# Kernel tuning notes

Measured on AMD Instinct MI355X. Metric: run time of the kernel, lower is better.

## Reference

```python
import jax, jax.numpy as jnp
import numpy as np

B, L, N, D = 128, 256, 64, 1024  # batch, text_len, img_num, feat size (text=obj=place=D)


def masked_softmax(logits, mask=None):
    # matches MaskedSoftmax(dim=1): softmax over last axis, then renormalize by mask
    dist = jax.nn.softmax(logits, axis=-1)
    if mask is None:
        return dist
    dist = dist * mask
    return dist / jnp.sum(dist, axis=-1, keepdims=True)


def setup_inputs() -> dict:
    key = jax.random.key(0)
    ks = jax.random.split(key, 32)
    s = lambda d: 1.0 / np.sqrt(d)
    inp = {
        'text_feat': jax.random.normal(ks[0], (B, D), jnp.float32),
        'text_feats': jax.random.normal(ks[1], (B, L, D), jnp.float32),
        'img_object_feat': jax.random.normal(ks[2], (B, D), jnp.float32),
        'img_object_feats': jax.random.normal(ks[3], (B, N, D), jnp.float32),
        'img_place_feat': jax.random.normal(ks[4], (B, D), jnp.float32),
        'img_place_feats': jax.random.normal(ks[5], (B, N, D), jnp.float32),
        'src_mask': (jax.random.uniform(ks[6], (B, L)) < 0.9).astype(jnp.float32).at[:, 0].set(1.0),
        # score vectors (nn.Linear(D,1,bias=False))
        'v_to': jax.random.uniform(ks[7], (D,), jnp.float32, -s(D), s(D)),
        'v_tp': jax.random.uniform(ks[8], (D,), jnp.float32, -s(D), s(D)),
        'v_io': jax.random.uniform(ks[9], (D,), jnp.float32, -s(D), s(D)),
        'v_ip': jax.random.uniform(ks[10], (D,), jnp.float32, -s(D), s(D)),
        # cross-modal projections (bias=False), torch layout [out,in]
        'W_t2o': jax.random.uniform(ks[11], (D, D), jnp.float32, -s(D), s(D)),
        'W_t2p': jax.random.uniform(ks[12], (D, D), jnp.float32, -s(D), s(D)),
        'W_o2t': jax.random.uniform(ks[13], (D, D), jnp.float32, -s(D), s(D)),
        'W_p2t': jax.random.uniform(ks[14], (D, D), jnp.float32, -s(D), s(D)),
        # self projections with bias
        'W_oo': jax.random.uniform(ks[15], (D, D), jnp.float32, -s(D), s(D)),
        'b_oo': jax.random.uniform(ks[16], (D,), jnp.float32, -s(D), s(D)),
        'W_pp': jax.random.uniform(ks[17], (D, D), jnp.float32, -s(D), s(D)),
        'b_pp': jax.random.uniform(ks[18], (D,), jnp.float32, -s(D), s(D)),
        'W_tot': jax.random.uniform(ks[19], (D, D), jnp.float32, -s(D), s(D)),
        'b_tot': jax.random.uniform(ks[20], (D,), jnp.float32, -s(D), s(D)),
        'W_tpt': jax.random.uniform(ks[21], (D, D), jnp.float32, -s(D), s(D)),
        'b_tpt': jax.random.uniform(ks[22], (D,), jnp.float32, -s(D), s(D)),
        # output linear: in = 2*D + D + D = 4D
        'W_out': jax.random.uniform(ks[23], (D, 4 * D), jnp.float32, -s(4 * D), s(4 * D)),
        'b_out': jax.random.uniform(ks[24], (D,), jnp.float32, -s(4 * D), s(4 * D)),
    }
    return inp


def _text_att_ctx(text_feat, img_feats, W_img2text, W_text, b_text, v):
    # additive attention of text over image regions
    e = jnp.tanh(jnp.einsum('bnd,td->bnt', img_feats, W_img2text)
                 + (text_feat @ W_text.T + b_text)[:, None, :])
    scores = jnp.einsum('bnt,t->bn', e, v)
    dist = masked_softmax(scores)
    return jnp.einsum('bn,bnd->bd', dist, img_feats)


def _img_att_ctx(img_feat, text_feats, W_text2img, W_img, b_img, v, mask):
    e = jnp.tanh(jnp.einsum('bld,id->bli', text_feats, W_text2img)
                 + (img_feat @ W_img.T + b_img)[:, None, :])
    scores = jnp.einsum('bli,i->bl', e, v)
    dist = masked_softmax(scores, mask)
    return jnp.einsum('bl,bld->bd', dist, text_feats)


def reference(text_feat, text_feats, img_object_feat, img_object_feats, img_place_feat,
              img_place_feats, src_mask, v_to, v_tp, v_io, v_ip, W_t2o, W_t2p, W_o2t,
              W_p2t, W_oo, b_oo, W_pp, b_pp, W_tot, b_tot, W_tpt, b_tpt, W_out, b_out):
    img_object_context = _text_att_ctx(text_feat, img_object_feats, W_o2t, W_tot, b_tot, v_to)
    img_place_context = _text_att_ctx(text_feat, img_place_feats, W_p2t, W_tpt, b_tpt, v_tp)
    text_object_context = _img_att_ctx(img_object_feat, text_feats, W_t2o, W_oo, b_oo, v_io, src_mask)
    text_place_context = _img_att_ctx(img_place_feat, text_feats, W_t2p, W_pp, b_pp, v_ip, src_mask)
    combined = jnp.concatenate([img_object_context, img_place_context,
                                text_object_context, text_place_context], axis=1)
    # dropout is identity at inference
    return combined @ W_out.T + b_out
```

## Files before the change

### kernel.cpp

```cpp
#include <hip/hip_runtime.h>
#include <hip/hip_bf16.h>

typedef __attribute__((ext_vector_type(8))) short bf16x8;
typedef __attribute__((ext_vector_type(4))) float f32x4;
typedef __attribute__((ext_vector_type(2))) long lx2;

__device__ __forceinline__ uint pack_bf16x2(float a, float b) {
    __hip_bfloat162 p = __float22bfloat162_rn(make_float2(a, b));
    union { __hip_bfloat162 h; uint u; } c; c.h = p; return c.u;
}

__device__ __forceinline__ float fast_tanh(float x) {
    float e = __expf(2.f * x);
    return 1.f - 2.f * __builtin_amdgcn_rcpf(e + 1.f);
}

__device__ __forceinline__ float wredmax(float v) {
    #pragma unroll
    for (int o = 32; o; o >>= 1) v = fmaxf(v, __shfl_xor(v, o, 64));
    return v;
}
__device__ __forceinline__ float wredsum(float v) {
    #pragma unroll
    for (int o = 32; o; o >>= 1) v += __shfl_xor(v, o, 64);
    return v;
}

__device__ __forceinline__ void gload16(const void* g, void* l) {
    __builtin_amdgcn_global_load_lds(
        (const __attribute__((address_space(1))) void*)g,
        (__attribute__((address_space(3))) void*)l, 16, 0, 0);
}

struct Cvt8Tab {
    const float* src[8];
    uchar* dst[8];
    unsigned cum[9];
};
struct CvtTab {
    const float* src[8];
    ushort* dst[8];
    unsigned cum[9];
};

__device__ __forceinline__ uint pk8(float4 v) {
    int r = __builtin_amdgcn_cvt_pk_fp8_f32(v.x, v.y, 0, false);
    r = __builtin_amdgcn_cvt_pk_fp8_f32(v.z, v.w, r, true);
    return (uint)r;
}

__global__ void cvt_all(Cvt8Tab t8, unsigned total8, CvtTab tb, unsigned totalb) {
    unsigned stride = gridDim.x * blockDim.x;
    unsigned total = total8 + totalb;
    for (unsigned i = blockIdx.x * blockDim.x + threadIdx.x; i < total; i += stride) {
        if (i < total8) {
            int j = 0;
            while (i >= t8.cum[j + 1]) ++j;
            unsigned o = i - t8.cum[j];
            unsigned row = o >> 6, c = o & 63, tt = c >> 2, pp = c & 3;
            const float* s0 = t8.src[j] + (size_t)row * 1024 + tt * 64 + pp * 8;
            float4 a0 = *(const float4*)(s0);
            float4 a1 = *(const float4*)(s0 + 4);
            float4 b0 = *(const float4*)(s0 + 32);
            float4 b1 = *(const float4*)(s0 + 36);
            uint4 ov;
            ov.x = pk8(a0); ov.y = pk8(a1); ov.z = pk8(b0); ov.w = pk8(b1);
            *reinterpret_cast<uint4*>(t8.dst[j] + (size_t)o * 16) = ov;
        } else {
            unsigned ii = i - total8;
            int j = 0;
            while (ii >= tb.cum[j + 1]) ++j;
            unsigned off = ii - tb.cum[j];
            float4 v = reinterpret_cast<const float4*>(tb.src[j])[off];
            uint2 o;
            o.x = pack_bf16x2(v.x, v.y);
            o.y = pack_bf16x2(v.z, v.w);
            reinterpret_cast<uint2*>(tb.dst[j])[off] = o;
        }
    }
}

struct PArgs {
    const uchar* A[2];
    const uchar* Wa[2];
    const uchar* Wb[2];
    const float* qa[2];
    const float* qb[2];
    const float* va[2];
    const float* vb[2];
    float* oa[2];
    float* ob[2];
};

__global__ __launch_bounds__(512, 1) void gemm_pipe8(PArgs Pi, PArgs Pt)
{
    extern __shared__ char smem[];

    const int tid = threadIdx.x;
    const int lane = tid & 63, wv = tid >> 6;
    const int wr = wv >> 2, wc = wv & 3;
    const int lrow = lane & 15, lk = lane >> 4;

    int id = blockIdx.x;
    const PArgs* P;
    int x, y, nmul, nbadd, bshift, brshift;
    if (id < 256) {
        P = &Pi; x = id & 63; y = id >> 6;
        nmul = 256; nbadd = 128; bshift = 6; brshift = 5;
    } else {
        P = &Pt; id -= 256; x = id & 127; y = id >> 7;
        nmul = 128; nbadd = 0; bshift = 8; brshift = 7;
    }
    const int br = x >> brshift;
    const int m0 = (x & ((1 << brshift) - 1)) << 8;
    const int na = y * nmul;
    const int nb = na + nbadd;

    const uchar* A  = P->A[br];
    const uchar* Wa = P->Wa[br];
    const uchar* Wb = P->Wb[br];

    const int rr = tid >> 2;
    const int c  = (tid & 3) ^ ((tid >> 3) & 3);
    const uchar* sA0 = A  + (size_t)(m0 + rr) * 1024 + c * 16;
    const uchar* sA1 = A  + (size_t)(m0 + 128 + rr) * 1024 + c * 16;
    const uchar* sW0 = Wa + (size_t)(na + rr) * 1024 + c * 16;
    const uchar* sW1 = Wb + (size_t)(nb + rr) * 1024 + c * 16;

    auto stage = [&](int t, int d) {
        char* b = smem + d * 32768 + tid * 16;
        size_t k = (size_t)t * 64;
        gload16(sA0 + k, b);
        gload16(sA1 + k, b + 8192);
        gload16(sW0 + k, b + 16384);
        gload16(sW1 + k, b + 24576);
    };

    auto rdA = [&](int d, int mi) -> lx2 {
        int row = wr * 128 + mi * 16 + lrow;
        return *(const lx2*)(smem + d * 32768 + row * 64 +
                             ((lk ^ ((row >> 1) & 3)) << 4));
    };
    auto rdB = [&](int d, int ni) -> lx2 {
        int row = wc * 64 + ni * 16 + lrow;
        return *(const lx2*)(smem + d * 32768 + 16384 + row * 64 +
                             ((lk ^ ((row >> 1) & 3)) << 4));
    };

    f32x4 acc[8][4];
    #pragma unroll
    for (int i = 0; i < 8; ++i)
        #pragma unroll
        for (int j = 0; j < 4; ++j) { f32x4 z = {0.f,0.f,0.f,0.f}; acc[i][j] = z; }

    stage(0, 0);
    asm volatile("s_waitcnt vmcnt(0)" ::: "memory");
    __syncthreads();

    auto body = [&](int t, int cur, int nxt, bool pf) {
        lx2 af[4], bfr[4];
        if (pf) stage(t + 1, nxt);
        #pragma unroll
        for (int ni = 0; ni < 4; ++ni) bfr[ni] = rdB(cur, ni);
        #pragma unroll
        for (int mi = 0; mi < 4; ++mi) af[mi] = rdA(cur, mi);
        __builtin_amdgcn_s_setprio(1);
        #pragma unroll
        for (int mi = 0; mi < 4; ++mi)
            #pragma unroll
            for (int ni = 0; ni < 4; ++ni) {
                acc[mi][ni] = __builtin_amdgcn_mfma_f32_16x16x32_fp8_fp8(af[mi][0], bfr[ni][0], acc[mi][ni], 0, 0, 0);
                acc[mi][ni] = __builtin_amdgcn_mfma_f32_16x16x32_fp8_fp8(af[mi][1], bfr[ni][1], acc[mi][ni], 0, 0, 0);
            }
        __builtin_amdgcn_s_setprio(0);
        #pragma unroll
        for (int mi = 0; mi < 4; ++mi) af[mi] = rdA(cur, mi + 4);
        __builtin_amdgcn_s_setprio(1);
        #pragma unroll
        for (int mi = 0; mi < 4; ++mi)
            #pragma unroll
            for (int ni = 0; ni < 4; ++ni) {
                acc[mi + 4][ni] = __builtin_amdgcn_mfma_f32_16x16x32_fp8_fp8(af[mi][0], bfr[ni][0], acc[mi + 4][ni], 0, 0, 0);
                acc[mi + 4][ni] = __builtin_amdgcn_mfma_f32_16x16x32_fp8_fp8(af[mi][1], bfr[ni][1], acc[mi + 4][ni], 0, 0, 0);
            }
        __builtin_amdgcn_s_setprio(0);
        asm volatile("s_waitcnt vmcnt(0)" ::: "memory");
        __syncthreads();
    };

    #pragma unroll 1
    for (int tt = 0; tt < 8; ++tt) {
        body(2 * tt,     0, 1, true);
        body(2 * tt + 1, 1, 0, tt < 7);
    }

    const float* qsrc = (wc < 2) ? P->qa[br] : P->qb[br];
    const float* vsrc = (wc < 2) ? P->va[br] : P->vb[br];
    float* osrc       = (wc < 2) ? P->oa[br] : P->ob[br];
    const int nbase0 = ((wc < 2) ? na : nb) + (wc & 1) * 64;
    #pragma unroll
    for (int mi = 0; mi < 8; ++mi) {
        int mbase = m0 + wr * 128 + mi * 16;
        int bb = mbase >> bshift;
        const float* qrow = qsrc + (size_t)bb * 1024;
        float part[4] = {0.f, 0.f, 0.f, 0.f};
        #pragma unroll
        for (int ni = 0; ni < 4; ++ni) {
            int nn = nbase0 + ni * 16 + lrow;
            float qn = qrow[nn], vn = vsrc[nn];
            #pragma unroll
            for (int r2 = 0; r2 < 4; ++r2)
                part[r2] += fast_tanh(acc[mi][ni][r2] + qn) * vn;
        }
        #pragma unroll
        for (int off = 1; off < 16; off <<= 1)
            #pragma unroll
            for (int r2 = 0; r2 < 4; ++r2)
                part[r2] += __shfl_xor(part[r2], off, 64);
        if (lrow == 0) {
            #pragma unroll
            for (int r2 = 0; r2 < 4; ++r2)
                atomicAdd(&osrc[mbase + lk * 4 + r2], part[r2]);
        }
    }
}

struct QArgs {
    const ushort* A[4];
    const ushort* W[4];
    const float* bias[4];
    float* out[4];
};

__global__ __launch_bounds__(256, 2) void gemm_q(QArgs Q, int kchunk)
{
    __shared__ char smemq[32768];
    char* As = smemq;
    char* Ws = smemq + 16384;

    const int tid = threadIdx.x;
    const int lane = tid & 63, wv = tid >> 6, wr = wv >> 1, wc = wv & 1;
    const int lrow = lane & 15, lk = lane >> 4;
    const int n0 = blockIdx.y << 7;
    const int nkt = kchunk >> 6;
    const int ktbase = blockIdx.z * nkt;

    const ushort* A = Q.A[blockIdx.x];
    const ushort* W = Q.W[blockIdx.x];

    f32x4 acc[4][4];
    #pragma unroll
    for (int i = 0; i < 4; ++i)
        #pragma unroll
        for (int j = 0; j < 4; ++j) { f32x4 z = {0.f,0.f,0.f,0.f}; acc[i][j] = z; }

    const int srow = tid >> 3;
    const int g = (tid & 7) ^ (srow & 7);
    const ushort* pA = A + (size_t)srow * 1024 + (size_t)ktbase * 64 + g * 8;
    const ushort* pW = W + (size_t)(n0 + srow) * 1024 + (size_t)ktbase * 64 + g * 8;

    for (int t = 0; t < nkt; ++t) {
        #pragma unroll
        for (int j = 0; j < 4; ++j)
            gload16(pA + (size_t)j * 32768 + (size_t)t * 64, As + j * 4096 + tid * 16);
        #pragma unroll
        for (int j = 0; j < 4; ++j)
            gload16(pW + (size_t)j * 32768 + (size_t)t * 64, Ws + j * 4096 + tid * 16);
        __syncthreads();
        #pragma unroll
        for (int ks = 0; ks < 2; ++ks) {
            bf16x8 af[4], bfr[4];
            const int q = ks * 4 + lk;
            #pragma unroll
            for (int mi = 0; mi < 4; ++mi) {
                int row = wr * 64 + mi * 16 + lrow;
                af[mi] = *(const bf16x8*)(As + row * 128 + ((q ^ (row & 7)) << 4));
            }
            #pragma unroll
            for (int ni = 0; ni < 4; ++ni) {
                int row = wc * 64 + ni * 16 + lrow;
                bfr[ni] = *(const bf16x8*)(Ws + row * 128 + ((q ^ (row & 7)) << 4));
            }
            #pragma unroll
            for (int mi = 0; mi < 4; ++mi)
                #pragma unroll
                for (int ni = 0; ni < 4; ++ni)
                    acc[mi][ni] = __builtin_amdgcn_mfma_f32_16x16x32_bf16(af[mi], bfr[ni], acc[mi][ni], 0, 0, 0);
        }
        __syncthreads();
    }

    float* out = Q.out[blockIdx.x];
    const float* bias = Q.bias[blockIdx.x];
    #pragma unroll
    for (int mi = 0; mi < 4; ++mi) {
        int mrow0 = wr * 64 + mi * 16 + lk * 4;
        #pragma unroll
        for (int ni = 0; ni < 4; ++ni) {
            int n = n0 + wc * 64 + ni * 16 + lrow;
            float bv = (blockIdx.z == 0) ? bias[n] : 0.f;
            #pragma unroll
            for (int r = 0; r < 4; ++r)
                atomicAdd(&out[(size_t)(mrow0 + r) * 1024 + n], acc[mi][ni][r] + bv);
        }
    }
}

__global__ __launch_bounds__(256, 2) void gemm_fin(
    const ushort* A, const ushort* W, const float* bias, float* out, int K, int kchunk)
{
    __shared__ char smemf[32768];
    char* As = smemf;
    char* Ws = smemf + 16384;

    const int tid = threadIdx.x;
    const int lane = tid & 63, wv = tid >> 6, wr = wv >> 1, wc = wv & 1;
    const int lrow = lane & 15, lk = lane >> 4;
    const int n0 = blockIdx.y << 7;
    const int nkt = kchunk >> 6;
    const int ktbase = blockIdx.z * nkt;

    f32x4 acc[4][4];
    #pragma unroll
    for (int i = 0; i < 4; ++i)
        #pragma unroll
        for (int j = 0; j < 4; ++j) { f32x4 z = {0.f,0.f,0.f,0.f}; acc[i][j] = z; }

    const int srow = tid >> 3;
    const int g = (tid & 7) ^ (srow & 7);
    const ushort* pA = A + (size_t)srow * K + ktbase * 64 + g * 8;
    const ushort* pW = W + (size_t)(n0 + srow) * K + ktbase * 64 + g * 8;

    for (int t = 0; t < nkt; ++t) {
        #pragma unroll
        for (int j = 0; j < 4; ++j)
            gload16(pA + (size_t)j * 32 * K + (size_t)t * 64, As + j * 4096 + tid * 16);
        #pragma unroll
        for (int j = 0; j < 4; ++j)
            gload16(pW + (size_t)j * 32 * K + (size_t)t * 64, Ws + j * 4096 + tid * 16);
        __syncthreads();
        #pragma unroll
        for (int ks = 0; ks < 2; ++ks) {
            bf16x8 af[4], bfr[4];
            const int q = ks * 4 + lk;
            #pragma unroll
            for (int mi = 0; mi < 4; ++mi) {
                int row = wr * 64 + mi * 16 + lrow;
                af[mi] = *(const bf16x8*)(As + row * 128 + ((q ^ (row & 7)) << 4));
            }
            #pragma unroll
            for (int ni = 0; ni < 4; ++ni) {
                int row = wc * 64 + ni * 16 + lrow;
                bfr[ni] = *(const bf16x8*)(Ws + row * 128 + ((q ^ (row & 7)) << 4));
            }
            #pragma unroll
            for (int mi = 0; mi < 4; ++mi)
                #pragma unroll
                for (int ni = 0; ni < 4; ++ni)
                    acc[mi][ni] = __builtin_amdgcn_mfma_f32_16x16x32_bf16(af[mi], bfr[ni], acc[mi][ni], 0, 0, 0);
        }
        __syncthreads();
    }

    #pragma unroll
    for (int mi = 0; mi < 4; ++mi) {
        int mrow0 = wr * 64 + mi * 16 + lk * 4;
        #pragma unroll
        for (int ni = 0; ni < 4; ++ni) {
            int n = n0 + wc * 64 + ni * 16 + lrow;
            float bv = (blockIdx.z == 0) ? bias[n] : 0.f;
            #pragma unroll
            for (int r = 0; r < 4; ++r)
                atomicAdd(&out[(size_t)(mrow0 + r) * 1024 + n], acc[mi][ni][r] + bv);
        }
    }
}

__global__ void softmax_ctx(const float* __restrict__ tf,
                            const float* __restrict__ iof, const float* __restrict__ ipf,
                            const float* __restrict__ sc_to, const float* __restrict__ sc_tp,
                            const float* __restrict__ sc_io, const float* __restrict__ sc_ip,
                            const float* __restrict__ mask, ushort* __restrict__ combined)
{
    int b = blockIdx.x, y = blockIdx.y;
    int tid = threadIdx.x, lane = tid & 63, wv = tid >> 6;
    if (y >= 2) {
        int brn = y - 2;
        const float* A  = brn ? ipf : iof;
        const float* sc = brn ? sc_ip : sc_io;
        __shared__ float dist[64];
        if (tid < 64) {
            float s  = sc[b * 64 + tid];
            float mx = wredmax(s);
            float e  = __expf(s - mx);
            float sm = wredsum(e);
            dist[tid] = e / sm;
        }
        __syncthreads();
        int d0 = tid * 4;
        float a0 = 0, a1 = 0, a2 = 0, a3 = 0;
        const float* base = A + (size_t)b * 64 * 1024 + d0;
        #pragma unroll 4
        for (int n = 0; n < 64; ++n) {
            float w = dist[n];
            float4 t = *(const float4*)(base + (size_t)n * 1024);
            a0 += w * t.x; a1 += w * t.y; a2 += w * t.z; a3 += w * t.w;
        }
        uint2 o;
        o.x = pack_bf16x2(a0, a1);
        o.y = pack_bf16x2(a2, a3);
        *(uint2*)(combined + (size_t)b * 4096 + brn * 1024 + d0) = o;
    } else {
        __shared__ float d3[256], d4[256], red[8];
        float s3 = sc_to[b * 256 + tid], s4 = sc_tp[b * 256 + tid], m = mask[b * 256 + tid];
        float m3 = wredmax(s3), m4 = wredmax(s4);
        if (lane == 0) { red[wv] = m3; red[4 + wv] = m4; }
        __syncthreads();
        m3 = fmaxf(fmaxf(red[0], red[1]), fmaxf(red[2], red[3]));
        m4 = fmaxf(fmaxf(red[4], red[5]), fmaxf(red[6], red[7]));
        float e3 = __expf(s3 - m3) * m, e4 = __expf(s4 - m4) * m;
        float t3 = wredsum(e3), t4 = wredsum(e4);
        __syncthreads();
        if (lane == 0) { red[wv] = t3; red[4 + wv] = t4; }
        __syncthreads();
        t3 = red[0] + red[1] + red[2] + red[3];
        t4 = red[4] + red[5] + red[6] + red[7];
        d3[tid] = e3 / t3; d4[tid] = e4 / t4;
        __syncthreads();
        int d0 = y * 512 + tid * 2;
        float a0 = 0, a1 = 0, c0 = 0, c1 = 0;
        const float* base = tf + (size_t)b * 256 * 1024 + d0;
        #pragma unroll 4
        for (int l = 0; l < 256; ++l) {
            float w3 = d3[l], w4 = d4[l];
            float2 t = *(const float2*)(base + (size_t)l * 1024);
            a0 += w3 * t.x; a1 += w3 * t.y;
            c0 += w4 * t.x; c1 += w4 * t.y;
        }
        *(uint*)(combined + (size_t)b * 4096 + 2048 + d0) = pack_bf16x2(a0, a1);
        *(uint*)(combined + (size_t)b * 4096 + 3072 + d0) = pack_bf16x2(c0, c1);
    }
}

extern "C" void kernel_launch(void* const* d_in, const int* in_sizes, int n_in,
                              void* d_out, int out_size, void* d_ws, size_t ws_size,
                              hipStream_t stream) {
    const float* text_feat        = (const float*)d_in[0];
    const float* text_feats       = (const float*)d_in[1];
    const float* img_object_feat  = (const float*)d_in[2];
    const float* img_object_feats = (const float*)d_in[3];
    const float* img_place_feat   = (const float*)d_in[4];
    const float* img_place_feats  = (const float*)d_in[5];
    const float* src_mask         = (const float*)d_in[6];
    const float* v_to  = (const float*)d_in[7];
    const float* v_tp  = (const float*)d_in[8];
    const float* v_io  = (const float*)d_in[9];
    const float* v_ip  = (const float*)d_in[10];
    const float* W_t2o = (const float*)d_in[11];
    const float* W_t2p = (const float*)d_in[12];
    const float* W_o2t = (const float*)d_in[13];
    const float* W_p2t = (const float*)d_in[14];
    const float* W_oo  = (const float*)d_in[15];
    const float* b_oo  = (const float*)d_in[16];
    const float* W_pp  = (const float*)d_in[17];
    const float* b_pp  = (const float*)d_in[18];
    const float* W_tot = (const float*)d_in[19];
    const float* b_tot = (const float*)d_in[20];
    const float* W_tpt = (const float*)d_in[21];
    const float* b_tpt = (const float*)d_in[22];
    const float* W_out = (const float*)d_in[23];
    const float* b_out = (const float*)d_in[24];

    char* p = (char*)d_ws;
    auto alloc = [&](size_t bytes) { char* r = p; p += (bytes + 255) & ~(size_t)255; return r; };
    ushort* wq_oo  = (ushort*)alloc((size_t)1024 * 1024 * 2);
    ushort* wq_pp  = (ushort*)alloc((size_t)1024 * 1024 * 2);
    ushort* wq_tot = (ushort*)alloc((size_t)1024 * 1024 * 2);
    ushort* wq_tpt = (ushort*)alloc((size_t)1024 * 1024 * 2);
    ushort* wb_out = (ushort*)alloc((size_t)1024 * 4096 * 2);
    ushort* tfq_bf  = (ushort*)alloc((size_t)128 * 1024 * 2);
    ushort* iofq_bf = (ushort*)alloc((size_t)128 * 1024 * 2);
    ushort* ipfq_bf = (ushort*)alloc((size_t)128 * 1024 * 2);
    uchar* w8_t2o = (uchar*)alloc((size_t)1024 * 1024);
    uchar* w8_t2p = (uchar*)alloc((size_t)1024 * 1024);
    uchar* w8_o2t = (uchar*)alloc((size_t)1024 * 1024);
    uchar* w8_p2t = (uchar*)alloc((size_t)1024 * 1024);
    uchar* tf8  = (uchar*)alloc((size_t)32768 * 1024);
    uchar* iof8 = (uchar*)alloc((size_t)8192 * 1024);
    uchar* ipf8 = (uchar*)alloc((size_t)8192 * 1024);
    float* q_tot = (float*)alloc((size_t)128 * 1024 * 4);
    float* q_tpt = (float*)alloc((size_t)128 * 1024 * 4);
    float* q_oo  = (float*)alloc((size_t)128 * 1024 * 4);
    float* q_pp  = (float*)alloc((size_t)128 * 1024 * 4);
    float* scores = (float*)alloc((size_t)(8192 * 2 + 32768 * 2) * 4);
    float* sc_io = scores, *sc_ip = scores + 8192, *sc_to = scores + 16384, *sc_tp = scores + 49152;
    ushort* comb_bf = (ushort*)alloc((size_t)128 * 4096 * 2);

    Cvt8Tab t8;
    const float* s8[7] = { W_t2o, W_t2p, W_o2t, W_p2t, text_feats, img_object_feats, img_place_feats };
    uchar* d8[7] = { w8_t2o, w8_t2p, w8_o2t, w8_p2t, tf8, iof8, ipf8 };
    unsigned n16[7] = { 65536, 65536, 65536, 65536, 2097152, 524288, 524288 };
    unsigned cum8 = 0;
    for (int i = 0; i < 7; ++i) { t8.src[i] = s8[i]; t8.dst[i] = d8[i]; t8.cum[i] = cum8; cum8 += n16[i]; }
    t8.src[7] = nullptr; t8.dst[7] = nullptr; t8.cum[7] = cum8; t8.cum[8] = cum8;

    CvtTab tb;
    const float* sb[8] = { W_oo, W_pp, W_tot, W_tpt, W_out, text_feat, img_object_feat, img_place_feat };
    ushort* db[8] = { wq_oo, wq_pp, wq_tot, wq_tpt, wb_out, tfq_bf, iofq_bf, ipfq_bf };
    unsigned nb4[8] = { 262144, 262144, 262144, 262144, 1048576, 32768, 32768, 32768 };
    unsigned cumb = 0;
    for (int i = 0; i < 8; ++i) { tb.src[i] = sb[i]; tb.dst[i] = db[i]; tb.cum[i] = cumb; cumb += nb4[i]; }
    tb.cum[8] = cumb;
    cvt_all<<<4096, 256, 0, stream>>>(t8, cum8, tb, cumb);

    hipMemsetAsync(q_tot, 0, (size_t)4 * 524288 + 327680, stream);
    hipMemsetAsync(d_out, 0, (size_t)128 * 1024 * 4, stream);

    QArgs qa;
    qa.A[0] = tfq_bf;  qa.W[0] = wq_tot; qa.bias[0] = b_tot; qa.out[0] = q_tot;
    qa.A[1] = tfq_bf;  qa.W[1] = wq_tpt; qa.bias[1] = b_tpt; qa.out[1] = q_tpt;
    qa.A[2] = iofq_bf; qa.W[2] = wq_oo;  qa.bias[2] = b_oo;  qa.out[2] = q_oo;
    qa.A[3] = ipfq_bf; qa.W[3] = wq_pp;  qa.bias[3] = b_pp;  qa.out[3] = q_pp;
    gemm_q<<<dim3(4, 8, 4), 256, 0, stream>>>(qa, 256);

    PArgs pi;
    pi.A[0] = iof8;   pi.Wa[0] = w8_o2t; pi.Wb[0] = w8_o2t;
    pi.qa[0] = q_tot; pi.qb[0] = q_tot;  pi.va[0] = v_to; pi.vb[0] = v_to;
    pi.oa[0] = sc_io; pi.ob[0] = sc_io;
    pi.A[1] = ipf8;   pi.Wa[1] = w8_p2t; pi.Wb[1] = w8_p2t;
    pi.qa[1] = q_tpt; pi.qb[1] = q_tpt;  pi.va[1] = v_tp; pi.vb[1] = v_tp;
    pi.oa[1] = sc_ip; pi.ob[1] = sc_ip;

    PArgs pt;
    pt.A[0] = tf8;    pt.Wa[0] = w8_t2o; pt.Wb[0] = w8_t2p;
    pt.qa[0] = q_oo;  pt.qb[0] = q_pp;   pt.va[0] = v_io; pt.vb[0] = v_ip;
    pt.oa[0] = sc_to; pt.ob[0] = sc_tp;
    pt.A[1] = pt.A[0]; pt.Wa[1] = pt.Wa[0]; pt.Wb[1] = pt.Wb[0];
    pt.qa[1] = pt.qa[0]; pt.qb[1] = pt.qb[0]; pt.va[1] = pt.va[0]; pt.vb[1] = pt.vb[0];
    pt.oa[1] = pt.oa[0]; pt.ob[1] = pt.ob[0];

    gemm_pipe8<<<dim3(1280), 512, 65536, stream>>>(pi, pt);

    softmax_ctx<<<dim3(128, 4), 256, 0, stream>>>(
        text_feats, img_object_feats, img_place_feats,
        sc_to, sc_tp, sc_io, sc_ip, src_mask, comb_bf);

    gemm_fin<<<dim3(1, 8, 16), 256, 0, stream>>>(comb_bf, wb_out, b_out, (float*)d_out, 4096, 256);
}
```

Before: 270.1 us.

## Halve FP8 GEMM M-tile to 128 rows and fold memsets into convert kernel

The fused FP8 score GEMM now uses 256-thread blocks with a 128x256 tile (4 waves in a 2x2 arrangement, each computing 64x128) instead of 512-thread blocks with a 256x256 tile. This doubles the grid and allows two blocks per CU through launch bounds and a smaller LDS footprint, aiming at better occupancy and latency hiding at the cost of lower operand reuse per block. Separately, the two hipMemsetAsync calls are removed and their zeroing is folded into the cvt_all kernel's grid-stride loop, which saves launch overhead.

Result: faster. 246.7 us (median of 2 runs) (-8.6%).

```diff
diff --git a/kernel.cpp b/kernel.cpp
--- a/kernel.cpp
+++ b/kernel.cpp
@@ -49,9 +49,10 @@
     return (uint)r;
 }
 
-__global__ void cvt_all(Cvt8Tab t8, unsigned total8, CvtTab tb, unsigned totalb) {
+__global__ void cvt_all(Cvt8Tab t8, unsigned total8, CvtTab tb, unsigned totalb,
+                        uint4* z1, unsigned n1, uint4* z2, unsigned n2) {
     unsigned stride = gridDim.x * blockDim.x;
-    unsigned total = total8 + totalb;
+    unsigned total = total8 + totalb + n1 + n2;
     for (unsigned i = blockIdx.x * blockDim.x + threadIdx.x; i < total; i += stride) {
         if (i < total8) {
             int j = 0;
@@ -66,7 +67,7 @@
             uint4 ov;
             ov.x = pk8(a0); ov.y = pk8(a1); ov.z = pk8(b0); ov.w = pk8(b1);
             *reinterpret_cast<uint4*>(t8.dst[j] + (size_t)o * 16) = ov;
-        } else {
+        } else if (i < total8 + totalb) {
             unsigned ii = i - total8;
             int j = 0;
             while (ii >= tb.cum[j + 1]) ++j;
@@ -76,6 +77,11 @@
             o.x = pack_bf16x2(v.x, v.y);
             o.y = pack_bf16x2(v.z, v.w);
             reinterpret_cast<uint2*>(tb.dst[j])[off] = o;
+        } else {
+            unsigned ii = i - total8 - totalb;
+            uint4 zz = {0u, 0u, 0u, 0u};
+            if (ii < n1) z1[ii] = zz;
+            else z2[ii - n1] = zz;
         }
     }
 }
@@ -92,27 +98,27 @@
     float* ob[2];
 };
 
-__global__ __launch_bounds__(512, 1) void gemm_pipe8(PArgs Pi, PArgs Pt)
+__global__ __launch_bounds__(256, 2) void gemm_pipe8(PArgs Pi, PArgs Pt)
 {
     extern __shared__ char smem[];
 
     const int tid = threadIdx.x;
     const int lane = tid & 63, wv = tid >> 6;
-    const int wr = wv >> 2, wc = wv & 3;
+    const int wr = wv >> 1, wc = wv & 1;
     const int lrow = lane & 15, lk = lane >> 4;
 
     int id = blockIdx.x;
     const PArgs* P;
     int x, y, nmul, nbadd, bshift, brshift;
-    if (id < 256) {
-        P = &Pi; x = id & 63; y = id >> 6;
-        nmul = 256; nbadd = 128; bshift = 6; brshift = 5;
+    if (id < 512) {
+        P = &Pi; x = id & 127; y = id >> 7;
+        nmul = 256; nbadd = 128; bshift = 6; brshift = 6;
     } else {
-        P = &Pt; id -= 256; x = id & 127; y = id >> 7;
-        nmul = 128; nbadd = 0; bshift = 8; brshift = 7;
+        P = &Pt; id -= 512; x = id & 255; y = id >> 8;
+        nmul = 128; nbadd = 0; bshift = 8; brshift = 8;
     }
     const int br = x >> brshift;
-    const int m0 = (x & ((1 << brshift) - 1)) << 8;
+    const int m0 = (x & ((1 << brshift) - 1)) << 7;
     const int na = y * nmul;
     const int nb = na + nbadd;
 
@@ -123,35 +129,39 @@
     const int rr = tid >> 2;
     const int c  = (tid & 3) ^ ((tid >> 3) & 3);
     const uchar* sA0 = A  + (size_t)(m0 + rr) * 1024 + c * 16;
-    const uchar* sA1 = A  + (size_t)(m0 + 128 + rr) * 1024 + c * 16;
+    const uchar* sA1 = A  + (size_t)(m0 + 64 + rr) * 1024 + c * 16;
     const uchar* sW0 = Wa + (size_t)(na + rr) * 1024 + c * 16;
-    const uchar* sW1 = Wb + (size_t)(nb + rr) * 1024 + c * 16;
+    const uchar* sW1 = Wa + (size_t)(na + 64 + rr) * 1024 + c * 16;
+    const uchar* sW2 = Wb + (size_t)(nb + rr) * 1024 + c * 16;
+    const uchar* sW3 = Wb + (size_t)(nb + 64 + rr) * 1024 + c * 16;
 
     auto stage = [&](int t, int d) {
-        char* b = smem + d * 32768 + tid * 16;
+        char* b = smem + d * 24576 + tid * 16;
         size_t k = (size_t)t * 64;
         gload16(sA0 + k, b);
-        gload16(sA1 + k, b + 8192);
-        gload16(sW0 + k, b + 16384);
-        gload16(sW1 + k, b + 24576);
+        gload16(sA1 + k, b + 4096);
+        gload16(sW0 + k, b + 8192);
+        gload16(sW1 + k, b + 12288);
+        gload16(sW2 + k, b + 16384);
+        gload16(sW3 + k, b + 20480);
     };
 
     auto rdA = [&](int d, int mi) -> lx2 {
-        int row = wr * 128 + mi * 16 + lrow;
-        return *(const lx2*)(smem + d * 32768 + row * 64 +
+        int row = wr * 64 + mi * 16 + lrow;
+        return *(const lx2*)(smem + d * 24576 + row * 64 +
                              ((lk ^ ((row >> 1) & 3)) << 4));
     };
     auto rdB = [&](int d, int ni) -> lx2 {
-        int row = wc * 64 + ni * 16 + lrow;
-        return *(const lx2*)(smem + d * 32768 + 16384 + row * 64 +
+        int row = wc * 128 + ni * 16 + lrow;
+        return *(const lx2*)(smem + d * 24576 + 8192 + row * 64 +
                              ((lk ^ ((row >> 1) & 3)) << 4));
     };
 
-    f32x4 acc[8][4];
-    #pragma unroll
-    for (int i = 0; i < 8; ++i)
-        #pragma unroll
-        for (int j = 0; j < 4; ++j) { f32x4 z = {0.f,0.f,0.f,0.f}; acc[i][j] = z; }
+    f32x4 acc[4][8];
+    #pragma unroll
+    for (int i = 0; i < 4; ++i)
+        #pragma unroll
+        for (int j = 0; j < 8; ++j) { f32x4 z = {0.f,0.f,0.f,0.f}; acc[i][j] = z; }
 
     stage(0, 0);
     asm volatile("s_waitcnt vmcnt(0)" ::: "memory");
@@ -161,9 +171,9 @@
         lx2 af[4], bfr[4];
         if (pf) stage(t + 1, nxt);
         #pragma unroll
+        for (int mi = 0; mi < 4; ++mi) af[mi] = rdA(cur, mi);
+        #pragma unroll
         for (int ni = 0; ni < 4; ++ni) bfr[ni] = rdB(cur, ni);
-        #pragma unroll
-        for (int mi = 0; mi < 4; ++mi) af[mi] = rdA(cur, mi);
         __builtin_amdgcn_s_setprio(1);
         #pragma unroll
         for (int mi = 0; mi < 4; ++mi)
@@ -174,14 +184,14 @@
             }
         __builtin_amdgcn_s_setprio(0);
         #pragma unroll
-        for (int mi = 0; mi < 4; ++mi) af[mi] = rdA(cur, mi + 4);
+        for (int ni = 0; ni < 4; ++ni) bfr[ni] = rdB(cur, ni + 4);
         __builtin_amdgcn_s_setprio(1);
         #pragma unroll
         for (int mi = 0; mi < 4; ++mi)
             #pragma unroll
             for (int ni = 0; ni < 4; ++ni) {
-                acc[mi + 4][ni] = __builtin_amdgcn_mfma_f32_16x16x32_fp8_fp8(af[mi][0], bfr[ni][0], acc[mi + 4][ni], 0, 0, 0);
-                acc[mi + 4][ni] = __builtin_amdgcn_mfma_f32_16x16x32_fp8_fp8(af[mi][1], bfr[ni][1], acc[mi + 4][ni], 0, 0, 0);
+                acc[mi][ni + 4] = __builtin_amdgcn_mfma_f32_16x16x32_fp8_fp8(af[mi][0], bfr[ni][0], acc[mi][ni + 4], 0, 0, 0);
+                acc[mi][ni + 4] = __builtin_amdgcn_mfma_f32_16x16x32_fp8_fp8(af[mi][1], bfr[ni][1], acc[mi][ni + 4], 0, 0, 0);
             }
         __builtin_amdgcn_s_setprio(0);
         asm volatile("s_waitcnt vmcnt(0)" ::: "memory");
@@ -194,19 +204,19 @@
         body(2 * tt + 1, 1, 0, tt < 7);
     }
 
-    const float* qsrc = (wc < 2) ? P->qa[br] : P->qb[br];
-    const float* vsrc = (wc < 2) ? P->va[br] : P->vb[br];
-    float* osrc       = (wc < 2) ? P->oa[br] : P->ob[br];
-    const int nbase0 = ((wc < 2) ? na : nb) + (wc & 1) * 64;
-    #pragma unroll
-    for (int mi = 0; mi < 8; ++mi) {
-        int mbase = m0 + wr * 128 + mi * 16;
+    const float* qsrc = wc ? P->qb[br] : P->qa[br];
+    const float* vsrc = wc ? P->vb[br] : P->va[br];
+    float* osrc       = wc ? P->ob[br] : P->oa[br];
+    const int nbase = wc ? nb : na;
+    #pragma unroll
+    for (int mi = 0; mi < 4; ++mi) {
+        int mbase = m0 + wr * 64 + mi * 16;
         int bb = mbase >> bshift;
         const float* qrow = qsrc + (size_t)bb * 1024;
         float part[4] = {0.f, 0.f, 0.f, 0.f};
         #pragma unroll
-        for (int ni = 0; ni < 4; ++ni) {
-            int nn = nbase0 + ni * 16 + lrow;
+        for (int ni = 0; ni < 8; ++ni) {
+            int nn = nbase + ni * 16 + lrow;
             float qn = qrow[nn], vn = vsrc[nn];
             #pragma unroll
             for (int r2 = 0; r2 < 4; ++r2)
@@ -511,10 +521,9 @@
     unsigned cumb = 0;
     for (int i = 0; i < 8; ++i) { tb.src[i] = sb[i]; tb.dst[i] = db[i]; tb.cum[i] = cumb; cumb += nb4[i]; }
     tb.cum[8] = cumb;
-    cvt_all<<<4096, 256, 0, stream>>>(t8, cum8, tb, cumb);
-
-    hipMemsetAsync(q_tot, 0, (size_t)4 * 524288 + 327680, stream);
-    hipMemsetAsync(d_out, 0, (size_t)128 * 1024 * 4, stream);
+
+    cvt_all<<<4096, 256, 0, stream>>>(t8, cum8, tb, cumb,
+                                      (uint4*)q_tot, 151552u, (uint4*)d_out, 32768u);
 
     QArgs qa;
     qa.A[0] = tfq_bf;  qa.W[0] = wq_tot; qa.bias[0] = b_tot; qa.out[0] = q_tot;
@@ -539,7 +548,7 @@
     pt.qa[1] = pt.qa[0]; pt.qb[1] = pt.qb[0]; pt.va[1] = pt.va[0]; pt.vb[1] = pt.vb[0];
     pt.oa[1] = pt.oa[0]; pt.ob[1] = pt.ob[0];
 
-    gemm_pipe8<<<dim3(1280), 512, 65536, stream>>>(pi, pt);
+    gemm_pipe8<<<dim3(2560), 256, 49152, stream>>>(pi, pt);
 
     softmax_ctx<<<dim3(128, 4), 256, 0, stream>>>(
         text_feats, img_object_feats, img_place_feats,
```
